# Performance work log

Measured on AMD Instinct MI355X. Metric: run time of the kernel, lower is better.

Reference implementation:

```python
import jax, jax.numpy as jnp
from jax import lax
import numpy as np

B = 8; L = 1024; D_MODEL = 128; N_LAYER = 4
D_INNER = 256; D_STATE = 16; D_CONV = 4; DT_RANK = 8  # ceil(128/16)
N_STATE = 2; EPS = 1e-5


def setup_inputs() -> dict:
    key = jax.random.key(0)
    ks = jax.random.split(key, 9)
    s = 0.02
    return {
        "x": jax.random.normal(ks[0], (B, L, D_MODEL), jnp.float32),
        "in_proj_w": jax.random.normal(ks[1], (N_LAYER, 2 * D_INNER, D_MODEL), jnp.float32) * s,
        "conv_w": jax.random.normal(ks[2], (N_LAYER, D_INNER, 1, D_CONV), jnp.float32) * s,
        "conv_b": jnp.zeros((N_LAYER, D_INNER), jnp.float32),
        "x_proj_w": jax.random.normal(ks[3], (N_LAYER, DT_RANK + 2 * D_STATE, D_INNER), jnp.float32) * s,
        "dt_proj_w": jax.random.normal(ks[4], (N_LAYER, D_INNER, DT_RANK), jnp.float32) * s,
        "dt_proj_b": jax.random.normal(ks[5], (N_LAYER, D_INNER), jnp.float32) * s,
        "A_log": jnp.log(jnp.tile(jnp.arange(1, D_STATE + 1, dtype=jnp.float32), (N_LAYER, D_INNER, 1))),
        "D_param": jnp.ones((N_LAYER, D_INNER), jnp.float32),
        "out_proj_w": jax.random.normal(ks[6], (N_LAYER, D_MODEL, D_INNER), jnp.float32) * s,
        "norm_w": jnp.ones((N_LAYER, D_MODEL), jnp.float32),
        "norm_f_w": jnp.ones((D_MODEL,), jnp.float32),
        "bn_gamma": jnp.ones((D_MODEL,), jnp.float32),
        "bn_beta": jnp.zeros((D_MODEL,), jnp.float32),
        "head_w": jax.random.normal(ks[7], (N_STATE, D_MODEL), jnp.float32) * s,
        "head_b": jnp.zeros((N_STATE,), jnp.float32),
    }


def _rmsnorm(x, w):
    return x * lax.rsqrt(jnp.mean(x * x, axis=-1, keepdims=True) + EPS) * w


def _selective_scan(u, delta, A, Bm, Cm, D):
    # u, delta: (b,l,d); A: (d,n); Bm, Cm: (b,l,n); D: (d,)
    deltaA = jnp.exp(delta[..., None] * A)                          # (b,l,d,n)
    deltaBu = delta[..., None] * Bm[:, :, None, :] * u[..., None]   # (b,l,d,n)

    def step(h, t):
        dA, dBu, c = t
        h = dA * h + dBu                                            # (b,d,n)
        return h, jnp.einsum('bdn,bn->bd', h, c)

    h0 = jnp.zeros((u.shape[0], u.shape[2], A.shape[1]), u.dtype)
    _, ys = lax.scan(step, h0, (jnp.moveaxis(deltaA, 1, 0),
                                jnp.moveaxis(deltaBu, 1, 0),
                                jnp.moveaxis(Cm, 1, 0)))
    return jnp.moveaxis(ys, 0, 1) + u * D                           # (b,l,d)


def _mamba_block(x, in_w, cw, cb, xp_w, dt_w, dt_b, A_log, Dp, out_w):
    xz = jnp.einsum('bld,ed->ble', x, in_w)                         # (b,l,2*d_inner)
    xs, res = jnp.split(xz, 2, axis=-1)
    # depthwise causal conv, kernel D_CONV, left pad D_CONV-1 (matches pad=3 + truncate)
    xc = lax.conv_general_dilated(jnp.transpose(xs, (0, 2, 1)), cw, (1,),
                                  [(D_CONV - 1, 0)],
                                  dimension_numbers=('NCH', 'OIH', 'NCH'),
                                  feature_group_count=D_INNER)
    xs = jax.nn.silu(jnp.transpose(xc + cb[None, :, None], (0, 2, 1)))
    dbc = jnp.einsum('bld,ed->ble', xs, xp_w)
    dlt, Bm, Cm = jnp.split(dbc, [DT_RANK, DT_RANK + D_STATE], axis=-1)
    delta = jax.nn.softplus(jnp.einsum('blr,dr->bld', dlt, dt_w) + dt_b)
    A = -jnp.exp(A_log)
    y = _selective_scan(xs, delta, A, Bm, Cm, Dp)
    y = y * jax.nn.silu(res)
    return jnp.einsum('ble,de->bld', y, out_w)


def reference(x, in_proj_w, conv_w, conv_b, x_proj_w, dt_proj_w, dt_proj_b,
              A_log, D_param, out_proj_w, norm_w, norm_f_w,
              bn_gamma, bn_beta, head_w, head_b):
    h = x
    for i in range(N_LAYER):
        h = h + _mamba_block(_rmsnorm(h, norm_w[i]), in_proj_w[i], conv_w[i],
                             conv_b[i], x_proj_w[i], dt_proj_w[i], dt_proj_b[i],
                             A_log[i], D_param[i], out_proj_w[i])
    h = _rmsnorm(h, norm_f_w)
    feat = h[:, -1, :]                                              # (b, d_model)
    # BatchNorm1d (training mode: batch stats, biased variance), ReLU, Dropout(eval)=id
    mu = jnp.mean(feat, axis=0)
    var = jnp.mean((feat - mu) ** 2, axis=0)
    feat = (feat - mu) * lax.rsqrt(var + EPS) * bn_gamma + bn_beta
    feat = jax.nn.relu(feat)
    return feat @ head_w.T + head_b                                 # (b, n_state)
```

## Files before the change

kernel.cpp:

```cpp
#include <hip/hip_runtime.h>
#include <cstddef>

#define LQ 1024
#define DM 128
#define DI 256
#define DSN 16
#define NB 8
#define ROWS (NB*LQ)
#define EPSF 1e-5f
#define CHUNK 16
#define NCHUNK (LQ/CHUNK)
#define NBLK (NB*NCHUNK)

typedef _Float16 f16;
typedef __attribute__((ext_vector_type(8))) _Float16 f16x8;
typedef __attribute__((ext_vector_type(4))) _Float16 f16x4;
typedef __attribute__((ext_vector_type(4))) float f32x4;

static __device__ __forceinline__ float sigmoid_f(float x) { return 1.f/(1.f+__expf(-x)); }
static __device__ __forceinline__ float softplus_f(float x) {
  return (x > 20.f) ? x : log1pf(__expf(x));
}

__global__ __launch_bounds__(256) void cvt_all(
    const float* __restrict__ a, const float* __restrict__ bsrc, const float* __restrict__ csrc,
    f16* __restrict__ oa, f16* __restrict__ ob, f16* __restrict__ oc)
{
  int i = blockIdx.x*256 + threadIdx.x;
  const int na = (4*2*DI*DM)/4;
  const int nb = (4*40*DI)/4;
  const int nc = (4*DM*DI)/4;
  const float* s; f16* o; int k;
  if (i < na)            { s = a;    o = oa; k = i; }
  else if (i < na+nb)    { s = bsrc; o = ob; k = i - na; }
  else if (i < na+nb+nc) { s = csrc; o = oc; k = i - na - nb; }
  else return;
  float4 v = ((const float4*)s)[k];
  f16x4 r; r.x=(f16)v.x; r.y=(f16)v.y; r.z=(f16)v.z; r.w=(f16)v.w;
  ((f16x4*)o)[k] = r;
}

__global__ __launch_bounds__(256) void layer_front(
    const float* __restrict__ src, const float* __restrict__ nw,
    const f16* __restrict__ Win,
    const float* __restrict__ cw, const float* __restrict__ cb,
    const f16* __restrict__ xpw,
    const float* __restrict__ A_log,
    const float* __restrict__ dtw, const float* __restrict__ dtb,
    f16* __restrict__ xs_out, float* __restrict__ dbc_out,
    float* __restrict__ S, float* __restrict__ sumdl_out)
{
  __shared__ __align__(16) f16 Ah[19][136];
  __shared__ __align__(16) f16 sXc[19][264];
  __shared__ __align__(16) f16 sXs[16][264];
  __shared__ __align__(16) float sDbc[16][40];
  const int bc = blockIdx.x;
  const int b = bc >> 6, ck = bc & (NCHUNK-1);
  const int t0 = ck*CHUNK;
  const int tid = threadIdx.x;
  const int l = tid & 63, w = tid >> 6;
  const int fr = l & 15, kg = l >> 4;

  {
    const int r = tid >> 3;
    const int seg = (tid & 7) * 16;
    const bool valid = (r < 19) && (ck > 0 || r >= 3);
    float4 v[4];
    float ss = 0.f;
    if (valid) {
      const float* hr = src + (size_t)(b*LQ + t0 - 3 + r)*DM + seg;
      #pragma unroll
      for (int j = 0; j < 4; ++j) {
        v[j] = *(const float4*)(hr + j*4);
        ss += v[j].x*v[j].x + v[j].y*v[j].y + v[j].z*v[j].z + v[j].w*v[j].w;
      }
    }
    ss += __shfl_xor(ss, 1); ss += __shfl_xor(ss, 2); ss += __shfl_xor(ss, 4);
    if (r < 19) {
      if (valid) {
        const float sc = rsqrtf(ss*(1.f/128.f) + EPSF);
        #pragma unroll
        for (int j = 0; j < 4; ++j) {
          float4 wv = *(const float4*)(nw + seg + j*4);
          f16x4 o;
          o.x=(f16)(v[j].x*sc*wv.x); o.y=(f16)(v[j].y*sc*wv.y);
          o.z=(f16)(v[j].z*sc*wv.z); o.w=(f16)(v[j].w*sc*wv.w);
          *(f16x4*)&Ah[r][seg + j*4] = o;
        }
      } else {
        #pragma unroll
        for (int j = 0; j < 4; ++j)
          *(f16x4*)&Ah[r][seg + j*4] = (f16x4){0,0,0,0};
      }
    }
  }
  __syncthreads();

  {
    f32x4 ax1[4], ax2[4];
    #pragma unroll
    for (int n = 0; n < 4; ++n) {
      ax1[n] = (f32x4){0.f,0.f,0.f,0.f};
      ax2[n] = (f32x4){0.f,0.f,0.f,0.f};
    }
    #pragma unroll
    for (int s = 0; s < 4; ++s) {
      f16x8 a1 = *(const f16x8*)&Ah[fr][s*32 + kg*8];
      f16x8 a2 = *(const f16x8*)&Ah[3 + fr][s*32 + kg*8];
      #pragma unroll
      for (int n = 0; n < 4; ++n) {
        f16x8 bx = *(const f16x8*)(Win + (size_t)(w*64 + n*16 + fr)*DM + s*32 + kg*8);
        ax1[n] = __builtin_amdgcn_mfma_f32_16x16x32_f16(a1, bx, ax1[n], 0, 0, 0);
        ax2[n] = __builtin_amdgcn_mfma_f32_16x16x32_f16(a2, bx, ax2[n], 0, 0, 0);
      }
    }
    #pragma unroll
    for (int n = 0; n < 4; ++n) {
      const int col = w*64 + n*16 + fr;
      #pragma unroll
      for (int j = 0; j < 4; ++j)
        sXc[3 + kg*4 + j][col] = (f16)ax2[n][j];
      if (kg == 0) {
        #pragma unroll
        for (int j = 0; j < 3; ++j)
          sXc[j][col] = (f16)ax1[n][j];
      }
    }
  }
  __syncthreads();

  {
    const int d = tid;
    const float4 cwv = *(const float4*)(cw + d*4);
    const float bias = cb[d];
    #pragma unroll 4
    for (int t = 0; t < CHUNK; ++t) {
      float a = bias + (float)sXc[t][d]*cwv.x + (float)sXc[t+1][d]*cwv.y
                     + (float)sXc[t+2][d]*cwv.z + (float)sXc[t+3][d]*cwv.w;
      float sv = a * sigmoid_f(a);
      f16 s16 = (f16)sv;
      sXs[t][d] = s16;
      xs_out[(size_t)(b*LQ + t0 + t)*DI + d] = s16;
    }
  }
  __syncthreads();

  if (w < 3) {
    const int col = w*16 + fr;
    f32x4 acc = (f32x4){0.f,0.f,0.f,0.f};
    #pragma unroll
    for (int s = 0; s < 8; ++s) {
      f16x8 bfv = (f16x8){0,0,0,0,0,0,0,0};
      if (col < 40) bfv = *(const f16x8*)(xpw + (size_t)col*DI + s*32 + kg*8);
      f16x8 afv = *(const f16x8*)&sXs[fr][s*32 + kg*8];
      acc = __builtin_amdgcn_mfma_f32_16x16x32_f16(afv, bfv, acc, 0, 0, 0);
    }
    if (col < 40) {
      #pragma unroll
      for (int j = 0; j < 4; ++j) {
        int row = kg*4 + j;
        sDbc[row][col] = acc[j];
        dbc_out[(size_t)(b*LQ + t0 + row)*40 + col] = acc[j];
      }
    }
  }
  __syncthreads();

  {
    const int d = tid;
    float A[16];
    #pragma unroll
    for (int n = 0; n < 16; ++n) A[n] = -__expf(A_log[d*16+n]);
    const float4 dw0 = *(const float4*)(dtw + d*8);
    const float4 dw1 = *(const float4*)(dtw + d*8 + 4);
    const float bt = dtb[d];
    float h[16] = {};
    float sdl = 0.f;
    for (int t = 0; t < CHUNK; ++t) {
      float xa = bt + sDbc[t][0]*dw0.x + sDbc[t][1]*dw0.y + sDbc[t][2]*dw0.z + sDbc[t][3]*dw0.w
                    + sDbc[t][4]*dw1.x + sDbc[t][5]*dw1.y + sDbc[t][6]*dw1.z + sDbc[t][7]*dw1.w;
      float dl = softplus_f(xa);
      float du = dl * (float)sXs[t][d];
      sdl += dl;
      #pragma unroll
      for (int n = 0; n < 16; ++n)
        h[n] = __expf(dl*A[n])*h[n] + du*sDbc[t][8+n];
    }
    float* Sp = S + ((size_t)bc*DI + d)*16;
    #pragma unroll
    for (int n = 0; n < 16; n += 4)
      *(float4*)(Sp+n) = make_float4(h[n],h[n+1],h[n+2],h[n+3]);
    sumdl_out[(size_t)bc*DI + d] = sdl;
  }
}

__global__ __launch_bounds__(256) void scan_p2(
    float* __restrict__ S, const float* __restrict__ sumdl,
    const float* __restrict__ A_log)
{
  int g = blockIdx.x*256 + threadIdx.x;
  int b = g >> 12;
  int dn = g & 4095;
  float A = -__expf(A_log[dn]);
  int d = dn >> 4;
  float H = 0.f;
  for (int c = 0; c < NCHUNK; ++c) {
    size_t cidx = (size_t)(b*NCHUNK + c)*DI + d;
    size_t idx = cidx*16 + (dn & 15);
    float Sv = S[idx];
    float P = __expf(A * sumdl[cidx]);
    S[idx] = H;
    H = P*H + Sv;
  }
}

__global__ __launch_bounds__(256) void layer_back(
    const float* __restrict__ src, const float* __restrict__ nw,
    const f16* __restrict__ Win,
    const f16* __restrict__ xs, const float* __restrict__ dbc,
    const float* __restrict__ A_log, const float* __restrict__ dtw,
    const float* __restrict__ dtb, const float* __restrict__ Dp,
    const float* __restrict__ Hinit, const f16* __restrict__ Wo,
    float* __restrict__ hout)
{
  __shared__ __align__(16) f16 Ah[16][136];
  __shared__ __align__(16) f16 sXs[16][264];
  __shared__ __align__(16) f16 sZ[16][264];
  __shared__ __align__(16) f16 sY[16][264];
  __shared__ __align__(16) float sDbc[16][40];
  const int bc = blockIdx.x;
  const int b = bc >> 6, ck = bc & (NCHUNK-1);
  const int t0 = ck*CHUNK;
  const int tid = threadIdx.x;
  const int l = tid & 63, w = tid >> 6;
  const int fr = l & 15, kg = l >> 4;

  {
    const int r = tid >> 4, col = (tid & 15) * 16;
    *(f16x8*)&sXs[r][col]   = *(const f16x8*)(xs + (size_t)(b*LQ + t0 + r)*DI + col);
    *(f16x8*)&sXs[r][col+8] = *(const f16x8*)(xs + (size_t)(b*LQ + t0 + r)*DI + col + 8);
  }
  for (int e = tid; e < 16*40; e += 256) {
    int t = e / 40, c = e % 40;
    sDbc[t][c] = dbc[(size_t)(b*LQ + t0 + t)*40 + c];
  }
  {
    const int r = tid >> 4;
    const int seg = (tid & 15) * 8;
    const float* hr = src + (size_t)(b*LQ + t0 + r)*DM + seg;
    float4 v0 = *(const float4*)(hr);
    float4 v1 = *(const float4*)(hr + 4);
    float ss = v0.x*v0.x+v0.y*v0.y+v0.z*v0.z+v0.w*v0.w
             + v1.x*v1.x+v1.y*v1.y+v1.z*v1.z+v1.w*v1.w;
    ss += __shfl_xor(ss, 1); ss += __shfl_xor(ss, 2);
    ss += __shfl_xor(ss, 4); ss += __shfl_xor(ss, 8);
    const float sc = rsqrtf(ss*(1.f/128.f) + EPSF);
    float4 w0 = *(const float4*)(nw + seg);
    float4 w1 = *(const float4*)(nw + seg + 4);
    f16x4 o0, o1;
    o0.x=(f16)(v0.x*sc*w0.x); o0.y=(f16)(v0.y*sc*w0.y);
    o0.z=(f16)(v0.z*sc*w0.z); o0.w=(f16)(v0.w*sc*w0.w);
    o1.x=(f16)(v1.x*sc*w1.x); o1.y=(f16)(v1.y*sc*w1.y);
    o1.z=(f16)(v1.z*sc*w1.z); o1.w=(f16)(v1.w*sc*w1.w);
    *(f16x4*)&Ah[r][seg]   = o0;
    *(f16x4*)&Ah[r][seg+4] = o1;
  }
  __syncthreads();

  {
    f32x4 az[4];
    #pragma unroll
    for (int n = 0; n < 4; ++n) az[n] = (f32x4){0.f,0.f,0.f,0.f};
    #pragma unroll
    for (int s = 0; s < 4; ++s) {
      f16x8 a = *(const f16x8*)&Ah[fr][s*32 + kg*8];
      #pragma unroll
      for (int n = 0; n < 4; ++n) {
        f16x8 bz = *(const f16x8*)(Win + (size_t)(DI + w*64 + n*16 + fr)*DM + s*32 + kg*8);
        az[n] = __builtin_amdgcn_mfma_f32_16x16x32_f16(a, bz, az[n], 0, 0, 0);
      }
    }
    #pragma unroll
    for (int n = 0; n < 4; ++n) {
      const int col = w*64 + n*16 + fr;
      #pragma unroll
      for (int j = 0; j < 4; ++j)
        sZ[kg*4 + j][col] = (f16)az[n][j];
    }
  }

  const int d = tid;
  float A[16];
  #pragma unroll
  for (int n = 0; n < 16; ++n) A[n] = -__expf(A_log[d*16+n]);
  float h[16];
  {
    const float* Hp = Hinit + ((size_t)bc*DI + d)*16;
    #pragma unroll
    for (int n = 0; n < 16; n += 4) {
      float4 v = *(const float4*)(Hp+n);
      h[n]=v.x; h[n+1]=v.y; h[n+2]=v.z; h[n+3]=v.w;
    }
  }
  const float4 dw0 = *(const float4*)(dtw + d*8);
  const float4 dw1 = *(const float4*)(dtw + d*8 + 4);
  const float bt = dtb[d];
  const float Dv = Dp[d];
  f16x8 bf[2][8];
  #pragma unroll
  for (int n = 0; n < 2; ++n)
    #pragma unroll
    for (int s = 0; s < 8; ++s)
      bf[n][s] = *(const f16x8*)(Wo + (size_t)(w*32 + n*16 + fr)*DI + s*32 + kg*8);
  __syncthreads();

  for (int t = 0; t < CHUNK; ++t) {
    float xa = bt + sDbc[t][0]*dw0.x + sDbc[t][1]*dw0.y + sDbc[t][2]*dw0.z + sDbc[t][3]*dw0.w
                  + sDbc[t][4]*dw1.x + sDbc[t][5]*dw1.y + sDbc[t][6]*dw1.z + sDbc[t][7]*dw1.w;
    float dl = softplus_f(xa);
    float uu = (float)sXs[t][d];
    float du = dl*uu;
    float pacc = uu*Dv;
    #pragma unroll
    for (int n = 0; n < 16; ++n) {
      h[n] = __expf(dl*A[n])*h[n] + du*sDbc[t][8+n];
      pacc += h[n]*sDbc[t][24+n];
    }
    float res = (float)sZ[t][d];
    sY[t][d] = (f16)(pacc * (res * sigmoid_f(res)));
  }
  __syncthreads();

  {
    f32x4 acc[2];
    acc[0] = (f32x4){0.f,0.f,0.f,0.f};
    acc[1] = (f32x4){0.f,0.f,0.f,0.f};
    #pragma unroll
    for (int s = 0; s < 8; ++s) {
      f16x8 afv = *(const f16x8*)&sY[fr][s*32 + kg*8];
      #pragma unroll
      for (int n = 0; n < 2; ++n)
        acc[n] = __builtin_amdgcn_mfma_f32_16x16x32_f16(afv, bf[n][s], acc[n], 0, 0, 0);
    }
    #pragma unroll
    for (int n = 0; n < 2; ++n) {
      const int col = w*32 + n*16 + fr;
      #pragma unroll
      for (int j = 0; j < 4; ++j) {
        const int row = kg*4 + j;
        const size_t gi = (size_t)(b*LQ + t0 + row)*DM + col;
        hout[gi] = acc[n][j] + src[gi];
      }
    }
  }
}

__global__ __launch_bounds__(256) void final_kernel(const float* __restrict__ h,
    const float* __restrict__ nfw, const float* __restrict__ gamma, const float* __restrict__ beta,
    const float* __restrict__ hw, const float* __restrict__ hb, float* __restrict__ out) {
  __shared__ float sf[8][128];
  __shared__ float sscale[8];
  int tid = threadIdx.x;
  for (int e = tid; e < 1024; e += 256) {
    int b = e >> 7, dd = e & 127;
    sf[b][dd] = h[((size_t)b*LQ + (LQ-1))*DM + dd];
  }
  __syncthreads();
  if (tid < 8) {
    float ss = 0.f;
    for (int dd = 0; dd < 128; ++dd) { float v = sf[tid][dd]; ss += v*v; }
    sscale[tid] = rsqrtf(ss/128.f + EPSF);
  }
  __syncthreads();
  for (int e = tid; e < 1024; e += 256) {
    int b = e >> 7, dd = e & 127;
    sf[b][dd] = sf[b][dd]*sscale[b]*nfw[dd];
  }
  __syncthreads();
  if (tid < 128) {
    float mu = 0.f;
    for (int b = 0; b < 8; ++b) mu += sf[b][tid];
    mu *= 0.125f;
    float var = 0.f;
    for (int b = 0; b < 8; ++b) { float dv = sf[b][tid]-mu; var += dv*dv; }
    var *= 0.125f;
    float rs = rsqrtf(var + EPSF);
    for (int b = 0; b < 8; ++b) {
      float v = (sf[b][tid]-mu)*rs*gamma[tid] + beta[tid];
      sf[b][tid] = v > 0.f ? v : 0.f;
    }
  }
  __syncthreads();
  if (tid < 16) {
    int b = tid >> 1, s = tid & 1;
    float acc = hb[s];
    for (int dd = 0; dd < 128; ++dd) acc += sf[b][dd]*hw[s*128+dd];
    out[b*2+s] = acc;
  }
}

extern "C" void kernel_launch(void* const* d_in, const int* in_sizes, int n_in,
                              void* d_out, int out_size, void* d_ws, size_t ws_size,
                              hipStream_t stream) {
  const float* x      = (const float*)d_in[0];
  const float* in_w   = (const float*)d_in[1];
  const float* conv_w = (const float*)d_in[2];
  const float* conv_b = (const float*)d_in[3];
  const float* xp_w   = (const float*)d_in[4];
  const float* dt_w   = (const float*)d_in[5];
  const float* dt_b   = (const float*)d_in[6];
  const float* A_log  = (const float*)d_in[7];
  const float* Dp     = (const float*)d_in[8];
  const float* out_w  = (const float*)d_in[9];
  const float* norm_w = (const float*)d_in[10];
  const float* norm_f = (const float*)d_in[11];
  const float* gamma  = (const float*)d_in[12];
  const float* beta   = (const float*)d_in[13];
  const float* head_w = (const float*)d_in[14];
  const float* head_b = (const float*)d_in[15];

  float* ws = (float*)d_ws;
  float* h     = ws;
  float* dbc   = h + (size_t)ROWS*DM;
  float* S     = dbc + (size_t)ROWS*40;
  float* sumdl = S + (size_t)NB*NCHUNK*DI*16;
  f16* xs     = (f16*)(sumdl + (size_t)NB*NCHUNK*DI);
  f16* wf_in  = xs + (size_t)ROWS*DI;
  f16* wf_xp  = wf_in + (size_t)4*2*DI*DM;
  f16* wf_out = wf_xp + (size_t)4*40*DI;

  cvt_all<<<424, 256, 0, stream>>>(in_w, xp_w, out_w, wf_in, wf_xp, wf_out);

  for (int layer = 0; layer < 4; ++layer) {
    const float* src = layer ? h : x;
    layer_front<<<NBLK, 256, 0, stream>>>(
        src, norm_w + (size_t)layer*DM, wf_in + (size_t)layer*2*DI*DM,
        conv_w + (size_t)layer*DI*4, conv_b + (size_t)layer*DI,
        wf_xp + (size_t)layer*40*DI, A_log + (size_t)layer*DI*DSN,
        dt_w + (size_t)layer*DI*8, dt_b + (size_t)layer*DI,
        xs, dbc, S, sumdl);
    scan_p2<<<NB*DI*DSN/256, 256, 0, stream>>>(S, sumdl, A_log + (size_t)layer*DI*DSN);
    layer_back<<<NBLK, 256, 0, stream>>>(
        src, norm_w + (size_t)layer*DM, wf_in + (size_t)layer*2*DI*DM,
        xs, dbc, A_log + (size_t)layer*DI*DSN,
        dt_w + (size_t)layer*DI*8, dt_b + (size_t)layer*DI,
        Dp + (size_t)layer*DI, S,
        wf_out + (size_t)layer*DM*DI, h);
  }
  final_kernel<<<1, 256, 0, stream>>>(h, norm_f, gamma, beta, head_w, head_b, (float*)d_out);
}
```

Measured before the change: 261.5 us.

## Halve scan chunk size to double block count, use exp2 and occupancy bounds

Reduces the time chunk per block from 16 to 8, doubling the number of blocks for the front and back layer kernels, and pads the MFMA tiles with zero rows. The exponentials switch to exp2f with A prescaled by log2(e), and launch bounds request 4 blocks per SM. The out-projection weights are now loaded inside the MFMA loop instead of being preloaded into registers. This aims to raise parallelism and occupancy on the sequential per-chunk scan, at the cost of half-empty MFMA tiles, a longer sequential carry pass in scan_p2 (128 chunks), and more workspace traffic.

```diff
diff --git a/kernel.cpp b/kernel.cpp
--- a/kernel.cpp
+++ b/kernel.cpp
@@ -8,9 +8,10 @@
 #define NB 8
 #define ROWS (NB*LQ)
 #define EPSF 1e-5f
-#define CHUNK 16
+#define CHUNK 8
 #define NCHUNK (LQ/CHUNK)
 #define NBLK (NB*NCHUNK)
+#define LOG2E 1.44269504f
 
 typedef _Float16 f16;
 typedef __attribute__((ext_vector_type(8))) _Float16 f16x8;
@@ -40,7 +41,7 @@
   ((f16x4*)o)[k] = r;
 }
 
-__global__ __launch_bounds__(256) void layer_front(
+__global__ __launch_bounds__(256, 4) void layer_front(
     const float* __restrict__ src, const float* __restrict__ nw,
     const f16* __restrict__ Win,
     const float* __restrict__ cw, const float* __restrict__ cb,
@@ -50,21 +51,25 @@
     f16* __restrict__ xs_out, float* __restrict__ dbc_out,
     float* __restrict__ S, float* __restrict__ sumdl_out)
 {
-  __shared__ __align__(16) f16 Ah[19][136];
-  __shared__ __align__(16) f16 sXc[19][264];
+  __shared__ __align__(16) f16 Ah[16][136];
+  __shared__ __align__(16) f16 sXc[11][264];
   __shared__ __align__(16) f16 sXs[16][264];
   __shared__ __align__(16) float sDbc[16][40];
   const int bc = blockIdx.x;
-  const int b = bc >> 6, ck = bc & (NCHUNK-1);
+  const int b = bc >> 7, ck = bc & (NCHUNK-1);
   const int t0 = ck*CHUNK;
   const int tid = threadIdx.x;
   const int l = tid & 63, w = tid >> 6;
   const int fr = l & 15, kg = l >> 4;
 
   {
+    const int row = 8 + (tid >> 5), col = (tid & 31) * 8;
+    *(f16x8*)&sXs[row][col] = (f16x8){0,0,0,0,0,0,0,0};
+  }
+  {
     const int r = tid >> 3;
     const int seg = (tid & 7) * 16;
-    const bool valid = (r < 19) && (ck > 0 || r >= 3);
+    const bool valid = (r < 11) && (ck > 0 || r >= 3);
     float4 v[4];
     float ss = 0.f;
     if (valid) {
@@ -76,7 +81,7 @@
       }
     }
     ss += __shfl_xor(ss, 1); ss += __shfl_xor(ss, 2); ss += __shfl_xor(ss, 4);
-    if (r < 19) {
+    if (r < 16) {
       if (valid) {
         const float sc = rsqrtf(ss*(1.f/128.f) + EPSF);
         #pragma unroll
@@ -97,33 +102,25 @@
   __syncthreads();
 
   {
-    f32x4 ax1[4], ax2[4];
-    #pragma unroll
-    for (int n = 0; n < 4; ++n) {
-      ax1[n] = (f32x4){0.f,0.f,0.f,0.f};
-      ax2[n] = (f32x4){0.f,0.f,0.f,0.f};
-    }
+    f32x4 ax[4];
+    #pragma unroll
+    for (int n = 0; n < 4; ++n) ax[n] = (f32x4){0.f,0.f,0.f,0.f};
     #pragma unroll
     for (int s = 0; s < 4; ++s) {
-      f16x8 a1 = *(const f16x8*)&Ah[fr][s*32 + kg*8];
-      f16x8 a2 = *(const f16x8*)&Ah[3 + fr][s*32 + kg*8];
+      f16x8 a = *(const f16x8*)&Ah[fr][s*32 + kg*8];
       #pragma unroll
       for (int n = 0; n < 4; ++n) {
         f16x8 bx = *(const f16x8*)(Win + (size_t)(w*64 + n*16 + fr)*DM + s*32 + kg*8);
-        ax1[n] = __builtin_amdgcn_mfma_f32_16x16x32_f16(a1, bx, ax1[n], 0, 0, 0);
-        ax2[n] = __builtin_amdgcn_mfma_f32_16x16x32_f16(a2, bx, ax2[n], 0, 0, 0);
+        ax[n] = __builtin_amdgcn_mfma_f32_16x16x32_f16(a, bx, ax[n], 0, 0, 0);
       }
     }
     #pragma unroll
     for (int n = 0; n < 4; ++n) {
       const int col = w*64 + n*16 + fr;
       #pragma unroll
-      for (int j = 0; j < 4; ++j)
-        sXc[3 + kg*4 + j][col] = (f16)ax2[n][j];
-      if (kg == 0) {
-        #pragma unroll
-        for (int j = 0; j < 3; ++j)
-          sXc[j][col] = (f16)ax1[n][j];
+      for (int j = 0; j < 4; ++j) {
+        const int row = kg*4 + j;
+        if (row < 11) sXc[row][col] = (f16)ax[n][j];
       }
     }
   }
@@ -133,7 +130,7 @@
     const int d = tid;
     const float4 cwv = *(const float4*)(cw + d*4);
     const float bias = cb[d];
-    #pragma unroll 4
+    #pragma unroll
     for (int t = 0; t < CHUNK; ++t) {
       float a = bias + (float)sXc[t][d]*cwv.x + (float)sXc[t+1][d]*cwv.y
                      + (float)sXc[t+2][d]*cwv.z + (float)sXc[t+3][d]*cwv.w;
@@ -158,9 +155,10 @@
     if (col < 40) {
       #pragma unroll
       for (int j = 0; j < 4; ++j) {
-        int row = kg*4 + j;
+        const int row = kg*4 + j;
         sDbc[row][col] = acc[j];
-        dbc_out[(size_t)(b*LQ + t0 + row)*40 + col] = acc[j];
+        if (row < 8)
+          dbc_out[(size_t)(b*LQ + t0 + row)*40 + col] = acc[j];
       }
     }
   }
@@ -170,12 +168,13 @@
     const int d = tid;
     float A[16];
     #pragma unroll
-    for (int n = 0; n < 16; ++n) A[n] = -__expf(A_log[d*16+n]);
+    for (int n = 0; n < 16; ++n) A[n] = -__expf(A_log[d*16+n]) * LOG2E;
     const float4 dw0 = *(const float4*)(dtw + d*8);
     const float4 dw1 = *(const float4*)(dtw + d*8 + 4);
     const float bt = dtb[d];
     float h[16] = {};
     float sdl = 0.f;
+    #pragma unroll
     for (int t = 0; t < CHUNK; ++t) {
       float xa = bt + sDbc[t][0]*dw0.x + sDbc[t][1]*dw0.y + sDbc[t][2]*dw0.z + sDbc[t][3]*dw0.w
                     + sDbc[t][4]*dw1.x + sDbc[t][5]*dw1.y + sDbc[t][6]*dw1.z + sDbc[t][7]*dw1.w;
@@ -184,7 +183,7 @@
       sdl += dl;
       #pragma unroll
       for (int n = 0; n < 16; ++n)
-        h[n] = __expf(dl*A[n])*h[n] + du*sDbc[t][8+n];
+        h[n] = exp2f(dl*A[n])*h[n] + du*sDbc[t][8+n];
     }
     float* Sp = S + ((size_t)bc*DI + d)*16;
     #pragma unroll
@@ -201,20 +200,20 @@
   int g = blockIdx.x*256 + threadIdx.x;
   int b = g >> 12;
   int dn = g & 4095;
-  float A = -__expf(A_log[dn]);
+  float A = -__expf(A_log[dn]) * LOG2E;
   int d = dn >> 4;
   float H = 0.f;
   for (int c = 0; c < NCHUNK; ++c) {
     size_t cidx = (size_t)(b*NCHUNK + c)*DI + d;
     size_t idx = cidx*16 + (dn & 15);
     float Sv = S[idx];
-    float P = __expf(A * sumdl[cidx]);
+    float P = exp2f(A * sumdl[cidx]);
     S[idx] = H;
     H = P*H + Sv;
   }
 }
 
-__global__ __launch_bounds__(256) void layer_back(
+__global__ __launch_bounds__(256, 4) void layer_back(
     const float* __restrict__ src, const float* __restrict__ nw,
     const f16* __restrict__ Win,
     const f16* __restrict__ xs, const float* __restrict__ dbc,
@@ -224,46 +223,55 @@
     float* __restrict__ hout)
 {
   __shared__ __align__(16) f16 Ah[16][136];
-  __shared__ __align__(16) f16 sXs[16][264];
-  __shared__ __align__(16) f16 sZ[16][264];
+  __shared__ __align__(16) f16 sXs[8][264];
+  __shared__ __align__(16) f16 sZ[8][264];
   __shared__ __align__(16) f16 sY[16][264];
-  __shared__ __align__(16) float sDbc[16][40];
+  __shared__ __align__(16) float sDbc[8][40];
   const int bc = blockIdx.x;
-  const int b = bc >> 6, ck = bc & (NCHUNK-1);
+  const int b = bc >> 7, ck = bc & (NCHUNK-1);
   const int t0 = ck*CHUNK;
   const int tid = threadIdx.x;
   const int l = tid & 63, w = tid >> 6;
   const int fr = l & 15, kg = l >> 4;
 
   {
-    const int r = tid >> 4, col = (tid & 15) * 16;
-    *(f16x8*)&sXs[r][col]   = *(const f16x8*)(xs + (size_t)(b*LQ + t0 + r)*DI + col);
-    *(f16x8*)&sXs[r][col+8] = *(const f16x8*)(xs + (size_t)(b*LQ + t0 + r)*DI + col + 8);
-  }
-  for (int e = tid; e < 16*40; e += 256) {
+    const int r = tid >> 5, col = (tid & 31) * 8;
+    *(f16x8*)&sXs[r][col] = *(const f16x8*)(xs + (size_t)(b*LQ + t0 + r)*DI + col);
+  }
+  for (int e = tid; e < 8*40; e += 256) {
     int t = e / 40, c = e % 40;
     sDbc[t][c] = dbc[(size_t)(b*LQ + t0 + t)*40 + c];
   }
   {
     const int r = tid >> 4;
     const int seg = (tid & 15) * 8;
-    const float* hr = src + (size_t)(b*LQ + t0 + r)*DM + seg;
-    float4 v0 = *(const float4*)(hr);
-    float4 v1 = *(const float4*)(hr + 4);
-    float ss = v0.x*v0.x+v0.y*v0.y+v0.z*v0.z+v0.w*v0.w
-             + v1.x*v1.x+v1.y*v1.y+v1.z*v1.z+v1.w*v1.w;
+    const bool valid = r < 8;
+    float4 v0 = make_float4(0,0,0,0), v1 = v0;
+    float ss = 0.f;
+    if (valid) {
+      const float* hr = src + (size_t)(b*LQ + t0 + r)*DM + seg;
+      v0 = *(const float4*)(hr);
+      v1 = *(const float4*)(hr + 4);
+      ss = v0.x*v0.x+v0.y*v0.y+v0.z*v0.z+v0.w*v0.w
+         + v1.x*v1.x+v1.y*v1.y+v1.z*v1.z+v1.w*v1.w;
+    }
     ss += __shfl_xor(ss, 1); ss += __shfl_xor(ss, 2);
     ss += __shfl_xor(ss, 4); ss += __shfl_xor(ss, 8);
-    const float sc = rsqrtf(ss*(1.f/128.f) + EPSF);
-    float4 w0 = *(const float4*)(nw + seg);
-    float4 w1 = *(const float4*)(nw + seg + 4);
-    f16x4 o0, o1;
-    o0.x=(f16)(v0.x*sc*w0.x); o0.y=(f16)(v0.y*sc*w0.y);
-    o0.z=(f16)(v0.z*sc*w0.z); o0.w=(f16)(v0.w*sc*w0.w);
-    o1.x=(f16)(v1.x*sc*w1.x); o1.y=(f16)(v1.y*sc*w1.y);
-    o1.z=(f16)(v1.z*sc*w1.z); o1.w=(f16)(v1.w*sc*w1.w);
-    *(f16x4*)&Ah[r][seg]   = o0;
-    *(f16x4*)&Ah[r][seg+4] = o1;
+    if (valid) {
+      const float sc = rsqrtf(ss*(1.f/128.f) + EPSF);
+      float4 w0 = *(const float4*)(nw + seg);
+      float4 w1 = *(const float4*)(nw + seg + 4);
+      f16x4 o0, o1;
+      o0.x=(f16)(v0.x*sc*w0.x); o0.y=(f16)(v0.y*sc*w0.y);
+      o0.z=(f16)(v0.z*sc*w0.z); o0.w=(f16)(v0.w*sc*w0.w);
+      o1.x=(f16)(v1.x*sc*w1.x); o1.y=(f16)(v1.y*sc*w1.y);
+      o1.z=(f16)(v1.z*sc*w1.z); o1.w=(f16)(v1.w*sc*w1.w);
+      *(f16x4*)&Ah[r][seg]   = o0;
+      *(f16x4*)&Ah[r][seg+4] = o1;
+    } else {
+      *(f16x4*)&Ah[r][seg]   = (f16x4){0,0,0,0};
+      *(f16x4*)&Ah[r][seg+4] = (f16x4){0,0,0,0};
+    }
   }
   __syncthreads();
 
@@ -284,15 +292,17 @@
     for (int n = 0; n < 4; ++n) {
       const int col = w*64 + n*16 + fr;
       #pragma unroll
-      for (int j = 0; j < 4; ++j)
-        sZ[kg*4 + j][col] = (f16)az[n][j];
+      for (int j = 0; j < 4; ++j) {
+        const int row = kg*4 + j;
+        if (row < 8) sZ[row][col] = (f16)az[n][j];
+      }
     }
   }
 
   const int d = tid;
   float A[16];
   #pragma unroll
-  for (int n = 0; n < 16; ++n) A[n] = -__expf(A_log[d*16+n]);
+  for (int n = 0; n < 16; ++n) A[n] = -__expf(A_log[d*16+n]) * LOG2E;
   float h[16];
   {
     const float* Hp = Hinit + ((size_t)bc*DI + d)*16;
@@ -306,14 +316,9 @@
   const float4 dw1 = *(const float4*)(dtw + d*8 + 4);
   const float bt = dtb[d];
   const float Dv = Dp[d];
-  f16x8 bf[2][8];
+  __syncthreads();
+
   #pragma unroll
-  for (int n = 0; n < 2; ++n)
-    #pragma unroll
-    for (int s = 0; s < 8; ++s)
-      bf[n][s] = *(const f16x8*)(Wo + (size_t)(w*32 + n*16 + fr)*DI + s*32 + kg*8);
-  __syncthreads();
-
   for (int t = 0; t < CHUNK; ++t) {
     float xa = bt + sDbc[t][0]*dw0.x + sDbc[t][1]*dw0.y + sDbc[t][2]*dw0.z + sDbc[t][3]*dw0.w
                   + sDbc[t][4]*dw1.x + sDbc[t][5]*dw1.y + sDbc[t][6]*dw1.z + sDbc[t][7]*dw1.w;
@@ -323,7 +328,7 @@
     float pacc = uu*Dv;
     #pragma unroll
     for (int n = 0; n < 16; ++n) {
-      h[n] = __expf(dl*A[n])*h[n] + du*sDbc[t][8+n];
+      h[n] = exp2f(dl*A[n])*h[n] + du*sDbc[t][8+n];
       pacc += h[n]*sDbc[t][24+n];
     }
     float res = (float)sZ[t][d];
@@ -339,8 +344,10 @@
     for (int s = 0; s < 8; ++s) {
       f16x8 afv = *(const f16x8*)&sY[fr][s*32 + kg*8];
       #pragma unroll
-      for (int n = 0; n < 2; ++n)
-        acc[n] = __builtin_amdgcn_mfma_f32_16x16x32_f16(afv, bf[n][s], acc[n], 0, 0, 0);
+      for (int n = 0; n < 2; ++n) {
+        f16x8 bfv = *(const f16x8*)(Wo + (size_t)(w*32 + n*16 + fr)*DI + s*32 + kg*8);
+        acc[n] = __builtin_amdgcn_mfma_f32_16x16x32_f16(afv, bfv, acc[n], 0, 0, 0);
+      }
     }
     #pragma unroll
     for (int n = 0; n < 2; ++n) {
@@ -348,8 +355,10 @@
       #pragma unroll
       for (int j = 0; j < 4; ++j) {
         const int row = kg*4 + j;
-        const size_t gi = (size_t)(b*LQ + t0 + row)*DM + col;
-        hout[gi] = acc[n][j] + src[gi];
+        if (row < 8) {
+          const size_t gi = (size_t)(b*LQ + t0 + row)*DM + col;
+          hout[gi] = acc[n][j] + src[gi];
+        }
       }
     }
   }
@@ -423,8 +432,8 @@
   float* h     = ws;
   float* dbc   = h + (size_t)ROWS*DM;
   float* S     = dbc + (size_t)ROWS*40;
-  float* sumdl = S + (size_t)NB*NCHUNK*DI*16;
-  f16* xs     = (f16*)(sumdl + (size_t)NB*NCHUNK*DI);
+  float* sumdl = S + (size_t)NBLK*DI*16;
+  f16* xs     = (f16*)(sumdl + (size_t)NBLK*DI);
   f16* wf_in  = xs + (size_t)ROWS*DI;
   f16* wf_xp  = wf_in + (size_t)4*2*DI*DM;
   f16* wf_out = wf_xp + (size_t)4*40*DI;
```

Result: slower. 327.7 us (+25.3%).

## Parallelize chunk-state scan across chunk groups and hoist parameter loads

Applied to the files above, without the earlier changes.

The inter-chunk scan kernel now splits the 64 chunks into 8 groups per thread block. Each group computes a local prefix of (P, S), the groups are combined through shared memory, and then each group rewrites its own states. This cuts the serial dependency chain from 64 steps to about 16 and launches more blocks. Per-thread parameter loads (dt weights, A_log, conv weights, x_proj weights, initial states, out_proj weights) are hoisted to kernel start so their latency overlaps the earlier phases, at the cost of more live registers. The exp calls are changed to exp2f with A prescaled by log2(e).

```diff
diff --git a/kernel.cpp b/kernel.cpp
--- a/kernel.cpp
+++ b/kernel.cpp
@@ -11,6 +11,7 @@
 #define CHUNK 16
 #define NCHUNK (LQ/CHUNK)
 #define NBLK (NB*NCHUNK)
+#define LOG2E 1.44269504f
 
 typedef _Float16 f16;
 typedef __attribute__((ext_vector_type(8))) _Float16 f16x8;
@@ -61,6 +62,26 @@
   const int l = tid & 63, w = tid >> 6;
   const int fr = l & 15, kg = l >> 4;
 
+  const float4 dw0 = *(const float4*)(dtw + tid*8);
+  const float4 dw1 = *(const float4*)(dtw + tid*8 + 4);
+  const float bt = dtb[tid];
+  float Araw[16];
+  #pragma unroll
+  for (int n = 0; n < 16; n += 4) {
+    float4 av = *(const float4*)(A_log + tid*16 + n);
+    Araw[n]=av.x; Araw[n+1]=av.y; Araw[n+2]=av.z; Araw[n+3]=av.w;
+  }
+  const float4 cwv = *(const float4*)(cw + tid*4);
+  const float cbias = cb[tid];
+  const int xcol = w*16 + fr;
+  const bool xpv = (w < 3) && (xcol < 40);
+  f16x8 xpf[8];
+  if (xpv) {
+    #pragma unroll
+    for (int s = 0; s < 8; ++s)
+      xpf[s] = *(const f16x8*)(xpw + (size_t)xcol*DI + s*32 + kg*8);
+  }
+
   {
     const int r = tid >> 3;
     const int seg = (tid & 7) * 16;
@@ -131,12 +152,10 @@
 
   {
     const int d = tid;
-    const float4 cwv = *(const float4*)(cw + d*4);
-    const float bias = cb[d];
     #pragma unroll 4
     for (int t = 0; t < CHUNK; ++t) {
-      float a = bias + (float)sXc[t][d]*cwv.x + (float)sXc[t+1][d]*cwv.y
-                     + (float)sXc[t+2][d]*cwv.z + (float)sXc[t+3][d]*cwv.w;
+      float a = cbias + (float)sXc[t][d]*cwv.x + (float)sXc[t+1][d]*cwv.y
+                      + (float)sXc[t+2][d]*cwv.z + (float)sXc[t+3][d]*cwv.w;
       float sv = a * sigmoid_f(a);
       f16 s16 = (f16)sv;
       sXs[t][d] = s16;
@@ -146,21 +165,19 @@
   __syncthreads();
 
   if (w < 3) {
-    const int col = w*16 + fr;
     f32x4 acc = (f32x4){0.f,0.f,0.f,0.f};
     #pragma unroll
     for (int s = 0; s < 8; ++s) {
-      f16x8 bfv = (f16x8){0,0,0,0,0,0,0,0};
-      if (col < 40) bfv = *(const f16x8*)(xpw + (size_t)col*DI + s*32 + kg*8);
+      f16x8 bfv = xpv ? xpf[s] : (f16x8){0,0,0,0,0,0,0,0};
       f16x8 afv = *(const f16x8*)&sXs[fr][s*32 + kg*8];
       acc = __builtin_amdgcn_mfma_f32_16x16x32_f16(afv, bfv, acc, 0, 0, 0);
     }
-    if (col < 40) {
+    if (xpv) {
       #pragma unroll
       for (int j = 0; j < 4; ++j) {
         int row = kg*4 + j;
-        sDbc[row][col] = acc[j];
-        dbc_out[(size_t)(b*LQ + t0 + row)*40 + col] = acc[j];
+        sDbc[row][xcol] = acc[j];
+        dbc_out[(size_t)(b*LQ + t0 + row)*40 + xcol] = acc[j];
       }
     }
   }
@@ -170,10 +187,7 @@
     const int d = tid;
     float A[16];
     #pragma unroll
-    for (int n = 0; n < 16; ++n) A[n] = -__expf(A_log[d*16+n]);
-    const float4 dw0 = *(const float4*)(dtw + d*8);
-    const float4 dw1 = *(const float4*)(dtw + d*8 + 4);
-    const float bt = dtb[d];
+    for (int n = 0; n < 16; ++n) A[n] = -__expf(Araw[n]) * LOG2E;
     float h[16] = {};
     float sdl = 0.f;
     for (int t = 0; t < CHUNK; ++t) {
@@ -184,7 +198,7 @@
       sdl += dl;
       #pragma unroll
       for (int n = 0; n < 16; ++n)
-        h[n] = __expf(dl*A[n])*h[n] + du*sDbc[t][8+n];
+        h[n] = exp2f(dl*A[n])*h[n] + du*sDbc[t][8+n];
     }
     float* Sp = S + ((size_t)bc*DI + d)*16;
     #pragma unroll
@@ -198,19 +212,43 @@
     float* __restrict__ S, const float* __restrict__ sumdl,
     const float* __restrict__ A_log)
 {
-  int g = blockIdx.x*256 + threadIdx.x;
-  int b = g >> 12;
-  int dn = g & 4095;
-  float A = -__expf(A_log[dn]);
-  int d = dn >> 4;
+  __shared__ float sP[8][32];
+  __shared__ float sS[8][32];
+  const int blk = blockIdx.x;
+  const int b = blk >> 7, dnblk = blk & 127;
+  const int tid = threadIdx.x;
+  const int g = tid >> 5;
+  const int dl = tid & 31;
+  const int dn = dnblk*32 + dl;
+  const int d = dn >> 4, n = dn & 15;
+  const float A = -__expf(A_log[dn]) * LOG2E;
+
+  float P[8], Sv[8];
+  float Pg = 1.f, Sg = 0.f;
+  #pragma unroll
+  for (int i = 0; i < 8; ++i) {
+    const int c = g*8 + i;
+    const size_t cidx = (size_t)(b*NCHUNK + c)*DI + d;
+    float p = exp2f(A * sumdl[cidx]);
+    float sv = S[cidx*16 + n];
+    P[i] = p; Sv[i] = sv;
+    Pg = p*Pg;
+    Sg = p*Sg + sv;
+  }
+  sP[g][dl] = Pg;
+  sS[g][dl] = Sg;
+  __syncthreads();
+
   float H = 0.f;
-  for (int c = 0; c < NCHUNK; ++c) {
-    size_t cidx = (size_t)(b*NCHUNK + c)*DI + d;
-    size_t idx = cidx*16 + (dn & 15);
-    float Sv = S[idx];
-    float P = __expf(A * sumdl[cidx]);
-    S[idx] = H;
-    H = P*H + Sv;
+  for (int j = 0; j < g; ++j)
+    H = sP[j][dl]*H + sS[j][dl];
+
+  #pragma unroll
+  for (int i = 0; i < 8; ++i) {
+    const int c = g*8 + i;
+    const size_t cidx = (size_t)(b*NCHUNK + c)*DI + d;
+    S[cidx*16 + n] = H;
+    H = P[i]*H + Sv[i];
   }
 }
 
@@ -235,6 +273,32 @@
   const int l = tid & 63, w = tid >> 6;
   const int fr = l & 15, kg = l >> 4;
 
+  const float4 dw0 = *(const float4*)(dtw + tid*8);
+  const float4 dw1 = *(const float4*)(dtw + tid*8 + 4);
+  const float bt = dtb[tid];
+  const float Dv = Dp[tid];
+  float Araw[16];
+  #pragma unroll
+  for (int n = 0; n < 16; n += 4) {
+    float4 av = *(const float4*)(A_log + tid*16 + n);
+    Araw[n]=av.x; Araw[n+1]=av.y; Araw[n+2]=av.z; Araw[n+3]=av.w;
+  }
+  float h[16];
+  {
+    const float* Hp = Hinit + ((size_t)bc*DI + tid)*16;
+    #pragma unroll
+    for (int n = 0; n < 16; n += 4) {
+      float4 v = *(const float4*)(Hp+n);
+      h[n]=v.x; h[n+1]=v.y; h[n+2]=v.z; h[n+3]=v.w;
+    }
+  }
+  f16x8 bf[2][8];
+  #pragma unroll
+  for (int n = 0; n < 2; ++n)
+    #pragma unroll
+    for (int s = 0; s < 8; ++s)
+      bf[n][s] = *(const f16x8*)(Wo + (size_t)(w*32 + n*16 + fr)*DI + s*32 + kg*8);
+
   {
     const int r = tid >> 4, col = (tid & 15) * 16;
     *(f16x8*)&sXs[r][col]   = *(const f16x8*)(xs + (size_t)(b*LQ + t0 + r)*DI + col);
@@ -288,30 +352,10 @@
         sZ[kg*4 + j][col] = (f16)az[n][j];
     }
   }
-
   const int d = tid;
   float A[16];
   #pragma unroll
-  for (int n = 0; n < 16; ++n) A[n] = -__expf(A_log[d*16+n]);
-  float h[16];
-  {
-    const float* Hp = Hinit + ((size_t)bc*DI + d)*16;
-    #pragma unroll
-    for (int n = 0; n < 16; n += 4) {
-      float4 v = *(const float4*)(Hp+n);
-      h[n]=v.x; h[n+1]=v.y; h[n+2]=v.z; h[n+3]=v.w;
-    }
-  }
-  const float4 dw0 = *(const float4*)(dtw + d*8);
-  const float4 dw1 = *(const float4*)(dtw + d*8 + 4);
-  const float bt = dtb[d];
-  const float Dv = Dp[d];
-  f16x8 bf[2][8];
-  #pragma unroll
-  for (int n = 0; n < 2; ++n)
-    #pragma unroll
-    for (int s = 0; s < 8; ++s)
-      bf[n][s] = *(const f16x8*)(Wo + (size_t)(w*32 + n*16 + fr)*DI + s*32 + kg*8);
+  for (int n = 0; n < 16; ++n) A[n] = -__expf(Araw[n]) * LOG2E;
   __syncthreads();
 
   for (int t = 0; t < CHUNK; ++t) {
@@ -323,7 +367,7 @@
     float pacc = uu*Dv;
     #pragma unroll
     for (int n = 0; n < 16; ++n) {
-      h[n] = __expf(dl*A[n])*h[n] + du*sDbc[t][8+n];
+      h[n] = exp2f(dl*A[n])*h[n] + du*sDbc[t][8+n];
       pacc += h[n]*sDbc[t][24+n];
     }
     float res = (float)sZ[t][d];
@@ -423,8 +467,8 @@
   float* h     = ws;
   float* dbc   = h + (size_t)ROWS*DM;
   float* S     = dbc + (size_t)ROWS*40;
-  float* sumdl = S + (size_t)NB*NCHUNK*DI*16;
-  f16* xs     = (f16*)(sumdl + (size_t)NB*NCHUNK*DI);
+  float* sumdl = S + (size_t)NBLK*DI*16;
+  f16* xs     = (f16*)(sumdl + (size_t)NBLK*DI);
   f16* wf_in  = xs + (size_t)ROWS*DI;
   f16* wf_xp  = wf_in + (size_t)4*2*DI*DM;
   f16* wf_out = wf_xp + (size_t)4*40*DI;
@@ -439,7 +483,7 @@
         wf_xp + (size_t)layer*40*DI, A_log + (size_t)layer*DI*DSN,
         dt_w + (size_t)layer*DI*8, dt_b + (size_t)layer*DI,
         xs, dbc, S, sumdl);
-    scan_p2<<<NB*DI*DSN/256, 256, 0, stream>>>(S, sumdl, A_log + (size_t)layer*DI*DSN);
+    scan_p2<<<NB*128, 256, 0, stream>>>(S, sumdl, A_log + (size_t)layer*DI*DSN);
     layer_back<<<NBLK, 256, 0, stream>>>(
         src, norm_w + (size_t)layer*DM, wf_in + (size_t)layer*2*DI*DM,
         xs, dbc, A_log + (size_t)layer*DI*DSN,
```

After: 290.2 us. +11.0%, slower.
